# Optimization experiments

Measured on AMD Instinct MI355X. Metric: run time of the kernel, lower is better.

The kernel has to match this reference:

```python
import jax, jax.numpy as jnp
import numpy as np

IN_FEATURES = 16384
OUT_FEATURES = 16384
NNZ = 1_000_000
BATCH = 256


def setup_inputs() -> dict:
    key = jax.random.key(0)
    k_x, k_w, k_b, k_r, k_c = jax.random.split(key, 5)
    x = jax.random.normal(k_x, (BATCH, IN_FEATURES), dtype=jnp.float32)
    weight_vals = jax.random.normal(k_w, (NNZ,), dtype=jnp.float32)
    bias = jax.random.normal(k_b, (OUT_FEATURES,), dtype=jnp.float32)
    rows = jax.random.randint(k_r, (NNZ,), 0, OUT_FEATURES, dtype=jnp.int32)
    cols = jax.random.randint(k_c, (NNZ,), 0, IN_FEATURES, dtype=jnp.int32)
    return {"x": x, "weight_vals": weight_vals, "bias": bias,
            "rows": rows, "cols": cols}


def reference(x, weight_vals, bias, rows, cols):
    # SparseLinear forward: y = x @ W^T + b, with W sparse COO of shape
    # [out_features, in_features]; (rows, cols) are W's nnz coordinates.
    # Per-edge contribution: x[:, col] * W[row, col], scattered into out[:, row].
    contrib = x[:, cols] * weight_vals  # [B, nnz]
    # segment-sum edges into output features: [nnz, B] -> [out, B]
    out = jax.ops.segment_sum(contrib.T, rows, num_segments=OUT_FEATURES).T
    return out + bias  # [B, out_features]
```

## Files before the change

### kernel.cpp

```cpp
#include <hip/hip_runtime.h>
#include <hip/hip_bf16.h>
#include <hip/hip_fp16.h>

#define BATCH_N 256
#define IN_F    16384
#define OUT_F   16384
#define CAP     128
#define NBUCK   256
#define CAPB    6656
#define EPB     2048
#define TBLK    1024
#define SENT    0xFFFFFFFFu

typedef unsigned int u32x4 __attribute__((ext_vector_type(4)));


__global__ void prep_kernel(const float* __restrict__ x,
                            __hip_bfloat16* __restrict__ xTh,
                            const int* __restrict__ rows,
                            const int* __restrict__ cols,
                            const float* __restrict__ vals, int nnz,
                            int* __restrict__ gcursor,
                            uint2* __restrict__ staging) {
    __shared__ int smem[64 * 65];
    int t = threadIdx.x;
    if (blockIdx.x < TBLK) {
        float* tile = (float*)smem;
        int bid = blockIdx.x;
        int i0 = (bid & 255) * 64;
        int b0 = (bid >> 8) * 64;
        int tx = t & 63, ty = t >> 6;
#pragma unroll
        for (int k = 0; k < 64; k += 4)
            tile[(ty + k) * 65 + tx] = x[(size_t)(b0 + ty + k) * IN_F + i0 + tx];
        __syncthreads();
        int h = b0 >> 7, j0 = b0 & 127;
#pragma unroll
        for (int k = 0; k < 64; k += 4) {
            int col = i0 + ty + k;
            xTh[((size_t)h * IN_F + col) * 128 + j0 + tx] =
                __float2bfloat16(tile[tx * 65 + ty + k]);
        }
    } else {
        int* hist = smem;
        int* base = smem + NBUCK;
        hist[t] = 0;
        __syncthreads();
        int i0 = (blockIdx.x - TBLK) * EPB;
        unsigned int pack[8], vb[8];
        int bk[8];
#pragma unroll
        for (int k = 0; k < 8; ++k) {
            int i = i0 + k * 256 + t;
            if (i < nnz) {
                int r = rows[i], c = cols[i];
                pack[k] = ((unsigned int)r << 14) | (unsigned int)c;
                vb[k] = __float_as_uint(vals[i]);
                bk[k] = r >> 6;
                atomicAdd(&hist[bk[k]], 1);
            } else bk[k] = -1;
        }
        __syncthreads();
        int hcnt = hist[t];
        int padded = (hcnt + 7) & ~7;
        base[t] = (padded > 0) ? atomicAdd(&gcursor[t], padded) : 0;
        __syncthreads();
        hist[t] = 0;
        __syncthreads();
#pragma unroll
        for (int k = 0; k < 8; ++k) {
            if (bk[k] >= 0) {
                int p = base[bk[k]] + atomicAdd(&hist[bk[k]], 1);
                if (p < CAPB)
                    staging[(size_t)bk[k] * CAPB + p] = make_uint2(pack[k], vb[k]);
            }
        }
        __syncthreads();
        for (int p = hcnt; p < padded; ++p) {
            int idx = base[t] + p;
            if (idx < CAPB)
                staging[(size_t)t * CAPB + idx] = make_uint2(SENT, 0u);
        }
    }
}


__global__ void bucket_scatter_kernel(const uint2* __restrict__ staging,
                                      const int* __restrict__ gcursor,
                                      unsigned int* __restrict__ edges,
                                      int* __restrict__ counts) {
    __shared__ int lcnt[64];
    __shared__ unsigned int lbin[64 * CAP];
    int b = blockIdx.x;
    int t = threadIdx.x;
    if (t < 64) lcnt[t] = 0;
    __syncthreads();
    int n = gcursor[b];
    if (n > CAPB) n = CAPB;
    const uint2* st = staging + (size_t)b * CAPB;
    for (int i = t; i < n; i += 256) {
        uint2 rec = st[i];
        if (rec.x != SENT) {
            int rl = (rec.x >> 14) & 63;
            int p = atomicAdd(&lcnt[rl], 1);
            if (p < CAP) {
                unsigned int col = rec.x & 16383u;
                __half hv = __float2half(__uint_as_float(rec.y));
                lbin[rl * CAP + p] = (col << 16) | (unsigned int)__half_as_ushort(hv);
            }
        }
    }
    __syncthreads();
    if (t < 64) {
        int c = lcnt[t];
        if (c > CAP) c = CAP;
        counts[b * 64 + t] = (c + 7) & ~7;
    }
    unsigned int* dst = edges + (size_t)b * 64 * CAP;
    for (int i4 = t; i4 < 64 * CAP / 4; i4 += 256) {
        int i = i4 * 4;
        int row = i >> 7;
        int slot = i & (CAP - 1);
        int c = lcnt[row];
        if (c > CAP) c = CAP;
        int lim = (c + 15) & ~15;
        if (slot < lim) {
            u32x4 v;
            v.x = (slot + 0 < c) ? lbin[i + 0] : 0u;
            v.y = (slot + 1 < c) ? lbin[i + 1] : 0u;
            v.z = (slot + 2 < c) ? lbin[i + 2] : 0u;
            v.w = (slot + 3 < c) ? lbin[i + 3] : 0u;
            __builtin_nontemporal_store(v, (u32x4*)(dst + i));
        }
    }
}


__global__ void accum_kernel(const unsigned int* __restrict__ xh0,
                             const unsigned int* __restrict__ edges,
                             const int*   __restrict__ counts,
                             const float* __restrict__ bias,
                             float* __restrict__ outT) {
    int blk = blockIdx.x;
    int h = blk & 1;
    int o = __builtin_amdgcn_readfirstlane(
        (int)((blk >> 1) * 4 + (threadIdx.x >> 6)));
    int t = threadIdx.x & 63;
    const unsigned int* xh = xh0 + (size_t)h * IN_F * 64;
    int n = counts[o];
    const unsigned int* el = edges + (size_t)o * CAP;
    float ax = 0.f, ay = 0.f;
    for (int j = 0; j < n; j += 8) {
        unsigned int e[8];
#pragma unroll
        for (int k = 0; k < 8; ++k) e[k] = el[j + k];
        unsigned int g[8];
#pragma unroll
        for (int k = 0; k < 8; ++k) {
            const unsigned int* p = xh + ((e[k] >> 16) << 6);
            g[k] = p[t];
        }
#pragma unroll
        for (int k = 0; k < 8; ++k) {
            float v = __half2float(__ushort_as_half((unsigned short)(e[k] & 0xffffu)));
            ax += __uint_as_float(g[k] << 16) * v;
            ay += __uint_as_float(g[k] & 0xffff0000u) * v;
        }
    }
    float bv = bias[o];
    unsigned long long w = ((unsigned long long)__float_as_uint(ay + bv) << 32)
                         | __float_as_uint(ax + bv);
    __builtin_nontemporal_store(w,
        (unsigned long long*)(outT + (size_t)o * 256 + h * 128 + 2 * t));
}


__global__ void transpose_out_kernel(const float* __restrict__ outT,
                                     float* __restrict__ out) {
    __shared__ float tile[64][65];
    int o0 = blockIdx.x * 64;
    int b0 = blockIdx.y * 64;
    int tx = threadIdx.x & 63;
    int ty = threadIdx.x >> 6;
#pragma unroll
    for (int k = 0; k < 64; k += 4)
        tile[ty + k][tx] =
            __builtin_nontemporal_load(&outT[(size_t)(o0 + ty + k) * BATCH_N + (b0 + tx)]);
    __syncthreads();
#pragma unroll
    for (int k = 0; k < 64; k += 4)
        __builtin_nontemporal_store(tile[tx][ty + k],
            &out[(size_t)(b0 + ty + k) * OUT_F + (o0 + tx)]);
}

extern "C" void kernel_launch(void* const* d_in, const int* in_sizes, int n_in,
                              void* d_out, int out_size, void* d_ws, size_t ws_size,
                              hipStream_t stream) {
    const float* x     = (const float*)d_in[0];
    const float* wvals = (const float*)d_in[1];
    const float* bias  = (const float*)d_in[2];
    const int*   rows  = (const int*)d_in[3];
    const int*   cols  = (const int*)d_in[4];
    float* out = (float*)d_out;
    int nnz = in_sizes[1];

    const size_t MB = 1024 * 1024;
    char* ws = (char*)d_ws;
    __hip_bfloat16* xTh = (__hip_bfloat16*)(ws);
    float* outT    = (float*)(ws + 8 * MB);
    uint2* staging = (uint2*)(ws + 8 * MB);
    unsigned int* edges = (unsigned int*)(ws + 24 * MB);
    int*   gcursor = (int*)(ws + 32 * MB);
    int*   counts  = (int*)(ws + 32 * MB + 4096);

    hipMemsetAsync(gcursor, 0, NBUCK * sizeof(int), stream);

    int npart = (nnz + EPB - 1) / EPB;
    prep_kernel<<<TBLK + npart, 256, 0, stream>>>(x, xTh, rows, cols, wvals, nnz,
                                                  gcursor, staging);
    bucket_scatter_kernel<<<NBUCK, 256, 0, stream>>>(staging, gcursor, edges, counts);
    accum_kernel<<<OUT_F / 2, 256, 0, stream>>>((const unsigned int*)xTh, edges,
                                                counts, bias, outT);
    transpose_out_kernel<<<dim3(OUT_F / 64, BATCH_N / 64), 256, 0, stream>>>(outT, out);
}
```

Before: 148.2 us.

## Fuse bucket scatter into accumulation kernel using LDS-resident edge lists

Merges the bucket-scatter and accumulation kernels: each block bins one staging bucket into shared memory and then its four waves accumulate sixteen output rows each, reading edges from LDS with scalar broadcasts. This removes a kernel launch and the global write and re-read of the padded edge array. Staging is moved so it no longer aliases outT and is read with 128-bit loads. In exchange the grid shrinks to 512 blocks, so fewer waves are available to hide gather latency, and each bucket's staging data is read twice, once per batch half.

Measured after the change: 171.6 us. 15.8% more time.

```diff
diff --git a/kernel.cpp b/kernel.cpp
--- a/kernel.cpp
+++ b/kernel.cpp
@@ -85,28 +85,36 @@
 }
 
 
-__global__ void bucket_scatter_kernel(const uint2* __restrict__ staging,
-                                      const int* __restrict__ gcursor,
-                                      unsigned int* __restrict__ edges,
-                                      int* __restrict__ counts) {
+__global__ void accum_kernel(const unsigned int* __restrict__ xh0,
+                             const uint2* __restrict__ staging,
+                             const int*   __restrict__ gcursor,
+                             const float* __restrict__ bias,
+                             float* __restrict__ outT) {
     __shared__ int lcnt[64];
     __shared__ unsigned int lbin[64 * CAP];
-    int b = blockIdx.x;
+    int blk = blockIdx.x;
+    int b = blk >> 1;
+    int h = blk & 1;
     int t = threadIdx.x;
     if (t < 64) lcnt[t] = 0;
     __syncthreads();
     int n = gcursor[b];
     if (n > CAPB) n = CAPB;
-    const uint2* st = staging + (size_t)b * CAPB;
-    for (int i = t; i < n; i += 256) {
-        uint2 rec = st[i];
-        if (rec.x != SENT) {
-            int rl = (rec.x >> 14) & 63;
-            int p = atomicAdd(&lcnt[rl], 1);
-            if (p < CAP) {
-                unsigned int col = rec.x & 16383u;
-                __half hv = __float2half(__uint_as_float(rec.y));
-                lbin[rl * CAP + p] = (col << 16) | (unsigned int)__half_as_ushort(hv);
+    const u32x4* st4 = (const u32x4*)(staging + (size_t)b * CAPB);
+    for (int i = t; i < n / 2; i += 256) {
+        u32x4 rr = __builtin_nontemporal_load(st4 + i);
+#pragma unroll
+        for (int q = 0; q < 2; ++q) {
+            unsigned int key = q ? rr.z : rr.x;
+            unsigned int vbits = q ? rr.w : rr.y;
+            if (key != SENT) {
+                int rl = (key >> 14) & 63;
+                int p = atomicAdd(&lcnt[rl], 1);
+                if (p < CAP) {
+                    unsigned int col = key & 16383u;
+                    __half hv = __float2half(__uint_as_float(vbits));
+                    lbin[rl * CAP + p] = (col << 16) | (unsigned int)__half_as_ushort(hv);
+                }
             }
         }
     }
@@ -114,64 +122,50 @@
     if (t < 64) {
         int c = lcnt[t];
         if (c > CAP) c = CAP;
-        counts[b * 64 + t] = (c + 7) & ~7;
-    }
-    unsigned int* dst = edges + (size_t)b * 64 * CAP;
-    for (int i4 = t; i4 < 64 * CAP / 4; i4 += 256) {
-        int i = i4 * 4;
-        int row = i >> 7;
-        int slot = i & (CAP - 1);
-        int c = lcnt[row];
-        if (c > CAP) c = CAP;
-        int lim = (c + 15) & ~15;
-        if (slot < lim) {
-            u32x4 v;
-            v.x = (slot + 0 < c) ? lbin[i + 0] : 0u;
-            v.y = (slot + 1 < c) ? lbin[i + 1] : 0u;
-            v.z = (slot + 2 < c) ? lbin[i + 2] : 0u;
-            v.w = (slot + 3 < c) ? lbin[i + 3] : 0u;
-            __builtin_nontemporal_store(v, (u32x4*)(dst + i));
-        }
-    }
-}
-
-
-__global__ void accum_kernel(const unsigned int* __restrict__ xh0,
-                             const unsigned int* __restrict__ edges,
-                             const int*   __restrict__ counts,
-                             const float* __restrict__ bias,
-                             float* __restrict__ outT) {
-    int blk = blockIdx.x;
-    int h = blk & 1;
-    int o = __builtin_amdgcn_readfirstlane(
-        (int)((blk >> 1) * 4 + (threadIdx.x >> 6)));
-    int t = threadIdx.x & 63;
+        int lim = (c + 7) & ~7;
+        for (int p = c; p < lim; ++p) lbin[t * CAP + p] = 0u;
+        lcnt[t] = lim;
+    }
+    __syncthreads();
+    int w = t >> 6;
+    int lane = t & 63;
     const unsigned int* xh = xh0 + (size_t)h * IN_F * 64;
-    int n = counts[o];
-    const unsigned int* el = edges + (size_t)o * CAP;
-    float ax = 0.f, ay = 0.f;
-    for (int j = 0; j < n; j += 8) {
-        unsigned int e[8];
-#pragma unroll
-        for (int k = 0; k < 8; ++k) e[k] = el[j + k];
-        unsigned int g[8];
-#pragma unroll
-        for (int k = 0; k < 8; ++k) {
-            const unsigned int* p = xh + ((e[k] >> 16) << 6);
-            g[k] = p[t];
-        }
-#pragma unroll
-        for (int k = 0; k < 8; ++k) {
-            float v = __half2float(__ushort_as_half((unsigned short)(e[k] & 0xffffu)));
-            ax += __uint_as_float(g[k] << 16) * v;
-            ay += __uint_as_float(g[k] & 0xffff0000u) * v;
-        }
-    }
-    float bv = bias[o];
-    unsigned long long w = ((unsigned long long)__float_as_uint(ay + bv) << 32)
-                         | __float_as_uint(ax + bv);
-    __builtin_nontemporal_store(w,
-        (unsigned long long*)(outT + (size_t)o * 256 + h * 128 + 2 * t));
+    for (int rr = 0; rr < 16; ++rr) {
+        int rl = w * 16 + rr;
+        int o = b * 64 + rl;
+        int nn = __builtin_amdgcn_readfirstlane(lcnt[rl]);
+        float ax = 0.f, ay = 0.f;
+        for (int j = 0; j < nn; j += 8) {
+            uint4 ea = *(const uint4*)&lbin[rl * CAP + j];
+            uint4 eb = *(const uint4*)&lbin[rl * CAP + j + 4];
+            unsigned int e[8];
+            e[0] = __builtin_amdgcn_readfirstlane(ea.x);
+            e[1] = __builtin_amdgcn_readfirstlane(ea.y);
+            e[2] = __builtin_amdgcn_readfirstlane(ea.z);
+            e[3] = __builtin_amdgcn_readfirstlane(ea.w);
+            e[4] = __builtin_amdgcn_readfirstlane(eb.x);
+            e[5] = __builtin_amdgcn_readfirstlane(eb.y);
+            e[6] = __builtin_amdgcn_readfirstlane(eb.z);
+            e[7] = __builtin_amdgcn_readfirstlane(eb.w);
+            unsigned int g[8];
+#pragma unroll
+            for (int k = 0; k < 8; ++k) {
+                const unsigned int* p = xh + ((e[k] >> 16) << 6);
+                g[k] = p[lane];
+            }
+#pragma unroll
+            for (int k = 0; k < 8; ++k) {
+                float v = __half2float(__ushort_as_half((unsigned short)(e[k] & 0xffffu)));
+                ax += __uint_as_float(g[k] << 16) * v;
+                ay += __uint_as_float(g[k] & 0xffff0000u) * v;
+            }
+        }
+        float bv = bias[o];
+        unsigned long long wv = ((unsigned long long)__float_as_uint(ay + bv) << 32)
+                              | __float_as_uint(ax + bv);
+        __builtin_nontemporal_store(wv,
+            (unsigned long long*)(outT + (size_t)o * 256 + h * 128 + 2 * lane));
+    }
 }
 
 
@@ -208,18 +202,15 @@
     char* ws = (char*)d_ws;
     __hip_bfloat16* xTh = (__hip_bfloat16*)(ws);
     float* outT    = (float*)(ws + 8 * MB);
-    uint2* staging = (uint2*)(ws + 8 * MB);
-    unsigned int* edges = (unsigned int*)(ws + 24 * MB);
-    int*   gcursor = (int*)(ws + 32 * MB);
-    int*   counts  = (int*)(ws + 32 * MB + 4096);
+    uint2* staging = (uint2*)(ws + 24 * MB);
+    int*   gcursor = (int*)(ws + 38 * MB);
 
     hipMemsetAsync(gcursor, 0, NBUCK * sizeof(int), stream);
 
     int npart = (nnz + EPB - 1) / EPB;
     prep_kernel<<<TBLK + npart, 256, 0, stream>>>(x, xTh, rows, cols, wvals, nnz,
                                                   gcursor, staging);
-    bucket_scatter_kernel<<<NBUCK, 256, 0, stream>>>(staging, gcursor, edges, counts);
-    accum_kernel<<<OUT_F / 2, 256, 0, stream>>>((const unsigned int*)xTh, edges,
-                                                counts, bias, outT);
+    accum_kernel<<<NBUCK * 2, 256, 0, stream>>>((const unsigned int*)xTh, staging,
+                                                gcursor, bias, outT);
     transpose_out_kernel<<<dim3(OUT_F / 64, BATCH_N / 64), 256, 0, stream>>>(outT, out);
 }
```

## Fuse output transpose into accumulation kernel and vectorize staging reads

Applied to the files above, without the earlier changes.

The accumulation kernel now processes 16 output features per block, stages results in shared memory, and writes the final [batch, out] layout directly. This eliminates the intermediate transposed buffer and the separate transpose kernel launch. Stores are 16-byte segments of 64 bytes per row, which is less coalesced than the old transpose. The bucket scatter also reads staging records two at a time with nontemporal 16-byte loads.

After: 144.0 us. 1.03x faster.

```diff
diff --git a/kernel.cpp b/kernel.cpp
--- a/kernel.cpp
+++ b/kernel.cpp
@@ -13,6 +13,7 @@
 #define SENT    0xFFFFFFFFu
 
 typedef unsigned int u32x4 __attribute__((ext_vector_type(4)));
+typedef float f32x4 __attribute__((ext_vector_type(4)));
 
 
 __global__ void prep_kernel(const float* __restrict__ x,
@@ -97,16 +98,22 @@
     __syncthreads();
     int n = gcursor[b];
     if (n > CAPB) n = CAPB;
-    const uint2* st = staging + (size_t)b * CAPB;
-    for (int i = t; i < n; i += 256) {
-        uint2 rec = st[i];
-        if (rec.x != SENT) {
-            int rl = (rec.x >> 14) & 63;
-            int p = atomicAdd(&lcnt[rl], 1);
-            if (p < CAP) {
-                unsigned int col = rec.x & 16383u;
-                __half hv = __float2half(__uint_as_float(rec.y));
-                lbin[rl * CAP + p] = (col << 16) | (unsigned int)__half_as_ushort(hv);
+    const u32x4* st4 = (const u32x4*)(staging + (size_t)b * CAPB);
+    for (int i = t; i < n / 2; i += 256) {
+        u32x4 rr = __builtin_nontemporal_load(st4 + i);
+#pragma unroll
+        for (int q = 0; q < 2; ++q) {
+            unsigned int key = q ? rr.z : rr.x;
+            unsigned int vbits = q ? rr.w : rr.y;
+            if (key != SENT) {
+                int rl = (key >> 14) & 63;
+                int p = atomicAdd(&lcnt[rl], 1);
+                if (p < CAP) {
+                    unsigned int col = key & 16383u;
+                    __half hv = __float2half(__uint_as_float(vbits));
+                    lbin[rl * CAP + p] =
+                        (col << 16) | (unsigned int)__half_as_ushort(hv);
+                }
             }
         }
     }
@@ -140,57 +147,56 @@
                              const unsigned int* __restrict__ edges,
                              const int*   __restrict__ counts,
                              const float* __restrict__ bias,
-                             float* __restrict__ outT) {
+                             float* __restrict__ out) {
+    __shared__ float slab[128][17];
     int blk = blockIdx.x;
     int h = blk & 1;
-    int o = __builtin_amdgcn_readfirstlane(
-        (int)((blk >> 1) * 4 + (threadIdx.x >> 6)));
-    int t = threadIdx.x & 63;
+    int o0 = (blk >> 1) * 16;
+    int w = threadIdx.x >> 6;
+    int lane = threadIdx.x & 63;
     const unsigned int* xh = xh0 + (size_t)h * IN_F * 64;
-    int n = counts[o];
-    const unsigned int* el = edges + (size_t)o * CAP;
-    float ax = 0.f, ay = 0.f;
-    for (int j = 0; j < n; j += 8) {
-        unsigned int e[8];
-#pragma unroll
-        for (int k = 0; k < 8; ++k) e[k] = el[j + k];
-        unsigned int g[8];
-#pragma unroll
-        for (int k = 0; k < 8; ++k) {
-            const unsigned int* p = xh + ((e[k] >> 16) << 6);
-            g[k] = p[t];
-        }
-#pragma unroll
-        for (int k = 0; k < 8; ++k) {
-            float v = __half2float(__ushort_as_half((unsigned short)(e[k] & 0xffffu)));
-            ax += __uint_as_float(g[k] << 16) * v;
-            ay += __uint_as_float(g[k] & 0xffff0000u) * v;
-        }
-    }
-    float bv = bias[o];
-    unsigned long long w = ((unsigned long long)__float_as_uint(ay + bv) << 32)
-                         | __float_as_uint(ax + bv);
-    __builtin_nontemporal_store(w,
-        (unsigned long long*)(outT + (size_t)o * 256 + h * 128 + 2 * t));
-}
-
-
-__global__ void transpose_out_kernel(const float* __restrict__ outT,
-                                     float* __restrict__ out) {
-    __shared__ float tile[64][65];
-    int o0 = blockIdx.x * 64;
-    int b0 = blockIdx.y * 64;
-    int tx = threadIdx.x & 63;
-    int ty = threadIdx.x >> 6;
-#pragma unroll
-    for (int k = 0; k < 64; k += 4)
-        tile[ty + k][tx] =
-            __builtin_nontemporal_load(&outT[(size_t)(o0 + ty + k) * BATCH_N + (b0 + tx)]);
+#pragma unroll
+    for (int rr = 0; rr < 4; ++rr) {
+        int rl = w * 4 + rr;
+        int o = __builtin_amdgcn_readfirstlane(o0 + rl);
+        int n = counts[o];
+        const unsigned int* el = edges + (size_t)o * CAP;
+        float ax = 0.f, ay = 0.f;
+        for (int j = 0; j < n; j += 8) {
+            unsigned int e[8];
+#pragma unroll
+            for (int k = 0; k < 8; ++k) e[k] = el[j + k];
+            unsigned int g[8];
+#pragma unroll
+            for (int k = 0; k < 8; ++k) {
+                const unsigned int* p = xh + ((e[k] >> 16) << 6);
+                g[k] = p[lane];
+            }
+#pragma unroll
+            for (int k = 0; k < 8; ++k) {
+                float v = __half2float(__ushort_as_half((unsigned short)(e[k] & 0xffffu)));
+                ax += __uint_as_float(g[k] << 16) * v;
+                ay += __uint_as_float(g[k] & 0xffff0000u) * v;
+            }
+        }
+        float bv = bias[o];
+        slab[2 * lane + 0][rl] = ax + bv;
+        slab[2 * lane + 1][rl] = ay + bv;
+    }
     __syncthreads();
 #pragma unroll
-    for (int k = 0; k < 64; k += 4)
-        __builtin_nontemporal_store(tile[tx][ty + k],
-            &out[(size_t)(b0 + ty + k) * OUT_F + (o0 + tx)]);
+    for (int it = 0; it < 2; ++it) {
+        int item = threadIdx.x + it * 256;
+        int bl = item >> 2;
+        int q = item & 3;
+        f32x4 v;
+        v.x = slab[bl][q * 4 + 0];
+        v.y = slab[bl][q * 4 + 1];
+        v.z = slab[bl][q * 4 + 2];
+        v.w = slab[bl][q * 4 + 3];
+        __builtin_nontemporal_store(v,
+            (f32x4*)(out + (size_t)(h * 128 + bl) * OUT_F + o0 + q * 4));
+    }
 }
 
 extern "C" void kernel_launch(void* const* d_in, const int* in_sizes, int n_in,
@@ -207,19 +213,17 @@
     const size_t MB = 1024 * 1024;
     char* ws = (char*)d_ws;
     __hip_bfloat16* xTh = (__hip_bfloat16*)(ws);
-    float* outT    = (float*)(ws + 8 * MB);
     uint2* staging = (uint2*)(ws + 8 * MB);
-    unsigned int* edges = (unsigned int*)(ws + 24 * MB);
-    int*   gcursor = (int*)(ws + 32 * MB);
-    int*   counts  = (int*)(ws + 32 * MB + 4096);
-
-    hipMemsetAsync(gcursor, 0, NBUCK * sizeof(int), stream);
+    unsigned int* edges = (unsigned int*)(ws + 22 * MB);
+    int*   gcursor = (int*)(ws + 30 * MB);
+    int*   counts  = (int*)(ws + 30 * MB + 4096);
+
+    (void)hipMemsetAsync(gcursor, 0, NBUCK * sizeof(int), stream);
 
     int npart = (nnz + EPB - 1) / EPB;
     prep_kernel<<<TBLK + npart, 256, 0, stream>>>(x, xTh, rows, cols, wvals, nnz,
                                                   gcursor, staging);
     bucket_scatter_kernel<<<NBUCK, 256, 0, stream>>>(staging, gcursor, edges, counts);
-    accum_kernel<<<OUT_F / 2, 256, 0, stream>>>((const unsigned int*)xTh, edges,
-                                                counts, bias, outT);
-    transpose_out_kernel<<<dim3(OUT_F / 64, BATCH_N / 64), 256, 0, stream>>>(outT, out);
-}
+    accum_kernel<<<(OUT_F / 16) * 2, 256, 0, stream>>>((const unsigned int*)xTh, edges,
+                                                       counts, bias, out);
+}
```
